# Optimization experiments

Measured on AMD Instinct MI355X. Metric: run time of the kernel, lower is better.

## Reference

```python
import jax, jax.numpy as jnp
import numpy as np

# Dims (Boltz MSA layer defaults)
S, N = 512, 384          # MSA depth, tokens
C_M, C_Z = 64, 128       # msa dim, pair dim
C_OPM = 32               # outer-product-mean hidden
H, DH = 8, 32            # heads, head_dim (H*DH == 256)
EPS = 1e-5


def _ln(x, w, b):
    mu = jnp.mean(x, axis=-1, keepdims=True)
    var = jnp.mean(jnp.square(x - mu), axis=-1, keepdims=True)
    return (x - mu) * jax.lax.rsqrt(var + EPS) * w + b


def setup_inputs() -> dict:
    key = jax.random.key(0)
    ks = iter(jax.random.split(key, 32))

    def p(*shape):
        return jax.random.normal(next(ks), shape, jnp.float32) * 0.02

    return {
        "m": jax.random.normal(next(ks), (1, S, N, C_M), jnp.float32),
        "z": jax.random.normal(next(ks), (1, N, N, C_Z), jnp.float32),
        # PairWeightedAveraging params
        "pwa_norm_m_w": jnp.ones((C_M,), jnp.float32),
        "pwa_norm_m_b": jnp.zeros((C_M,), jnp.float32),
        "pwa_norm_z_w": jnp.ones((C_Z,), jnp.float32),
        "pwa_norm_z_b": jnp.zeros((C_Z,), jnp.float32),
        "pwa_wm": p(C_M, H * DH),
        "pwa_wg": p(C_M, H * DH),
        "pwa_wz": p(C_Z, H),
        "pwa_wo": p(H * DH, C_M),
        # MSA Transition (SwiGLU, expansion 4)
        "tr_norm_w": jnp.ones((C_M,), jnp.float32),
        "tr_norm_b": jnp.zeros((C_M,), jnp.float32),
        "tr_w1": p(C_M, 4 * C_M),
        "tr_w2": p(C_M, 4 * C_M),
        "tr_w3": p(4 * C_M, C_M),
        # OuterProductMean params
        "opm_norm_w": jnp.ones((C_M,), jnp.float32),
        "opm_norm_b": jnp.zeros((C_M,), jnp.float32),
        "opm_wa": p(C_M, C_OPM),
        "opm_wb": p(C_M, C_OPM),
        "opm_wo": p(C_OPM * C_OPM, C_Z),
        "opm_bo": jnp.zeros((C_Z,), jnp.float32),
    }


def reference(m, z,
              pwa_norm_m_w, pwa_norm_m_b, pwa_norm_z_w, pwa_norm_z_b,
              pwa_wm, pwa_wg, pwa_wz, pwa_wo,
              tr_norm_w, tr_norm_b, tr_w1, tr_w2, tr_w3,
              opm_norm_w, opm_norm_b, opm_wa, opm_wb, opm_wo, opm_bo):
    m0 = m[0]   # [S, N, C_M]
    z0 = z[0]   # [N, N, C_Z]

    # --- Pair-weighted averaging (gated, per-head pair bias attention) ---
    mn = _ln(m0, pwa_norm_m_w, pwa_norm_m_b)
    zn = _ln(z0, pwa_norm_z_w, pwa_norm_z_b)
    b = zn @ pwa_wz                      # [N(i), N(j), H]
    w = jax.nn.softmax(b, axis=1)        # normalize over keys j
    v = (mn @ pwa_wm).reshape(S, N, H, DH)
    o = jnp.einsum('ijh,sjhd->sihd', w, v)           # [S, N, H, DH]
    g = jax.nn.sigmoid(mn @ pwa_wg).reshape(S, N, H, DH)
    pwa = (o * g).reshape(S, N, H * DH) @ pwa_wo     # [S, N, C_M]
    m1 = m0 + pwa

    # --- MSA transition (SwiGLU) ---
    tn = _ln(m1, tr_norm_w, tr_norm_b)
    m2 = m1 + (jax.nn.silu(tn @ tr_w1) * (tn @ tr_w2)) @ tr_w3

    # --- Outer product mean: MSA -> pair update ---
    on = _ln(m2, opm_norm_w, opm_norm_b)
    a = on @ opm_wa                      # [S, N, C]
    bb = on @ opm_wb                     # [S, N, C]
    op = jnp.einsum('sic,sjd->ijcd', a, bb) / S      # [N, N, C, C]
    zu = op.reshape(N, N, C_OPM * C_OPM) @ opm_wo + opm_bo
    z1 = z0 + zu

    return m2[None], z1[None]
```

## Files before the change

kernel.cpp:

```cpp
#include <hip/hip_runtime.h>
#include <hip/hip_bf16.h>

#define S_DIM 512
#define N_DIM 384
#define CM 64
#define CZ 128
#define HEADS 8
#define DH 32
#define HD 256

typedef __hip_bfloat16 bf16;
typedef long long i64;
typedef __attribute__((ext_vector_type(8))) short bf16x8;
typedef __attribute__((ext_vector_type(4))) float f32x4;

__device__ __forceinline__ float bf2f(bf16 x) { return __bfloat162float(x); }
__device__ __forceinline__ bf16 f2bf(float x) { return __float2bfloat16(x); }
__device__ __forceinline__ short f2bs(float x) {
  bf16 h = __float2bfloat16(x);
  return *reinterpret_cast<short*>(&h);
}

typedef __attribute__((address_space(3))) unsigned int lds_u32;
typedef __attribute__((address_space(1))) const unsigned int gbl_u32;
__device__ __forceinline__ void gl_lds16(const void* g, void* l) {
  __builtin_amdgcn_global_load_lds((gbl_u32*)g, (lds_u32*)l, 16, 0, 0);
}

__global__ __launch_bounds__(256) void k_wprep(const float* __restrict__ wm,
                                               const float* __restrict__ wg,
                                               const float* __restrict__ w1,
                                               const float* __restrict__ w2,
                                               const float* __restrict__ wpo,
                                               const float* __restrict__ w3,
                                               const float* __restrict__ wz,
                                               short* __restrict__ dst,
                                               short* __restrict__ wz_f) {
  if (blockIdx.x == 48) {
    int t = threadIdx.x;
    int ks = t >> 6, lane = t & 63, lg = lane >> 4, n = lane & 15;
    short out[8];
#pragma unroll
    for (int j = 0; j < 8; ++j) {
      int k = ks * 32 + lg * 8 + j;
      out[j] = (n < 8) ? f2bs(wz[k * 8 + n]) : (short)0;
    }
    *reinterpret_cast<float4*>(&wz_f[(size_t)t * 8]) =
        *reinterpret_cast<const float4*>(out);
    return;
  }
  int widx = blockIdx.x >> 3;
  const float* src;
  int N;
  if (widx == 0) { src = wm; N = 256; }
  else if (widx == 1) { src = wg; N = 256; }
  else if (widx == 2) { src = w1; N = 256; }
  else if (widx == 3) { src = w2; N = 256; }
  else if (widx == 4) { src = wpo; N = 64; }
  else { src = w3; N = 64; }
  int NF = N >> 4;
  int tg = ((blockIdx.x & 7) << 8) | threadIdx.x;
  int frag = tg >> 6, lane = tg & 63, lg = lane >> 4, l15 = lane & 15;
  int ks = frag / NF, nf = frag - ks * NF;
  short out[8];
#pragma unroll
  for (int j = 0; j < 8; ++j)
    out[j] = f2bs(src[(size_t)(ks * 32 + lg * 8 + j) * N + nf * 16 + l15]);
  *reinterpret_cast<float4*>(&dst[((size_t)widx << 14) + ((size_t)tg << 3)]) =
      *reinterpret_cast<const float4*>(out);
}

__global__ __launch_bounds__(256) void k_zb(const float* __restrict__ z,
                                            const float* __restrict__ w,
                                            const float* __restrict__ b,
                                            const short* __restrict__ wz_f,
                                            float* __restrict__ logits) {
  int blk = blockIdx.x;
  int i = blk / 6, j0 = (blk % 6) * 64;
  __shared__ __align__(16) char zl[16384];
  int t = threadIdx.x, wave = t >> 6, lane = t & 63;
  int lg = lane >> 4, l15 = lane & 15;
  float w0 = w[lane], w1 = w[lane + 64], b0 = b[lane], b1 = b[lane + 64];
  int rwb = wave * 16;
  const float* zbase = z + ((size_t)i * N_DIM + j0 + rwb) * CZ;
  for (int rr = 0; rr < 16; ++rr) {
    int row = rwb + rr;
    const float* zr = zbase + (size_t)rr * CZ;
    float v0 = zr[lane], v1 = zr[lane + 64];
    float s = v0 + v1, sq = v0 * v0 + v1 * v1;
#pragma unroll
    for (int off = 32; off; off >>= 1) {
      s += __shfl_xor(s, off);
      sq += __shfl_xor(sq, off);
    }
    float mu = s * (1.0f / CZ);
    float var = sq * (1.0f / CZ) - mu * mu;
    float rs = rsqrtf(var + 1e-5f);
    int sw = (row & 7) << 4;
    *reinterpret_cast<short*>(zl + row * 256 + ((2 * lane) ^ sw)) =
        f2bs((v0 - mu) * rs * w0 + b0);
    *reinterpret_cast<short*>(zl + row * 256 + ((2 * (lane + 64)) ^ sw)) =
        f2bs((v1 - mu) * rs * w1 + b1);
  }
  __syncthreads();
  f32x4 acc = (f32x4){0.f, 0.f, 0.f, 0.f};
  int arow = rwb + l15;
  int asw = (arow & 7) << 4;
#pragma unroll
  for (int ks = 0; ks < 4; ++ks) {
    bf16x8 a = *reinterpret_cast<const bf16x8*>(
        zl + arow * 256 + (((ks * 32 + lg * 8) * 2) ^ asw));
    bf16x8 bfr = *reinterpret_cast<const bf16x8*>(wz_f + ((size_t)ks * 64 + lane) * 8);
    acc = __builtin_amdgcn_mfma_f32_16x16x32_bf16(a, bfr, acc, 0, 0, 0);
  }
  if (l15 < 8) {
    int j = j0 + rwb + lg * 4;
    float4 o4;
    o4.x = acc[0]; o4.y = acc[1]; o4.z = acc[2]; o4.w = acc[3];
    *reinterpret_cast<float4*>(logits + ((size_t)i * 8 + l15) * N_DIM + j) = o4;
  }
}

__global__ __launch_bounds__(128) void k_softmax(const float* __restrict__ wb,
                                                 short* __restrict__ w8) {
  int row = blockIdx.x;
  int i = row >> 3, h = row & 7;
  const float* p = wb + (size_t)row * N_DIM;
  int t = threadIdx.x;
  float a0 = p[t], a1 = p[t + 128], a2 = p[t + 256];
  float mx = fmaxf(a0, fmaxf(a1, a2));
  __shared__ float red[2], red2[2];
#pragma unroll
  for (int off = 32; off; off >>= 1) mx = fmaxf(mx, __shfl_xor(mx, off));
  if ((t & 63) == 0) red[t >> 6] = mx;
  __syncthreads();
  mx = fmaxf(red[0], red[1]);
  float e0 = __expf(a0 - mx), e1 = __expf(a1 - mx), e2 = __expf(a2 - mx);
  float s = e0 + e1 + e2;
#pragma unroll
  for (int off = 32; off; off >>= 1) s += __shfl_xor(s, off);
  if ((t & 63) == 0) red2[t >> 6] = s;
  __syncthreads();
  float inv = 1.0f / (red2[0] + red2[1]);
  short* wr = w8 + ((size_t)h * N_DIM + i) * N_DIM;
  wr[t] = f2bs(e0 * inv);
  wr[t + 128] = f2bs(e1 * inv);
  wr[t + 256] = f2bs(e2 * inv);
}

__global__ __launch_bounds__(256, 1) void k_vgemm(const float* __restrict__ m0,
                                                  const float* __restrict__ nw,
                                                  const float* __restrict__ nb,
                                                  const short* __restrict__ wm_f,
                                                  short* __restrict__ vT) {
  int blk = blockIdx.x;
  int sblk = blk / 6, j0 = (blk % 6) * 64;
  __shared__ short vt[256 * 64];
  int t = threadIdx.x, wave = t >> 6, lane = t & 63;
  int lg = lane >> 4, l15 = lane & 15;
  size_t rb = (size_t)sblk * N_DIM + j0;
  int rw0 = wave * 16;
  const float* mrow = m0 + (rb + rw0 + l15) * CM;
  float4 x0 = *reinterpret_cast<const float4*>(mrow + lg * 8);
  float4 x1 = *reinterpret_cast<const float4*>(mrow + lg * 8 + 4);
  float4 x2 = *reinterpret_cast<const float4*>(mrow + 32 + lg * 8);
  float4 x3 = *reinterpret_cast<const float4*>(mrow + 32 + lg * 8 + 4);
  float s = x0.x + x0.y + x0.z + x0.w + x1.x + x1.y + x1.z + x1.w +
            x2.x + x2.y + x2.z + x2.w + x3.x + x3.y + x3.z + x3.w;
  float sq = x0.x * x0.x + x0.y * x0.y + x0.z * x0.z + x0.w * x0.w +
             x1.x * x1.x + x1.y * x1.y + x1.z * x1.z + x1.w * x1.w +
             x2.x * x2.x + x2.y * x2.y + x2.z * x2.z + x2.w * x2.w +
             x3.x * x3.x + x3.y * x3.y + x3.z * x3.z + x3.w * x3.w;
  s += __shfl_xor(s, 16); s += __shfl_xor(s, 32);
  sq += __shfl_xor(sq, 16); sq += __shfl_xor(sq, 32);
  float mu = s * (1.0f / CM);
  float var = sq * (1.0f / CM) - mu * mu;
  float rs = rsqrtf(var + 1e-5f);
  float4 g0 = *reinterpret_cast<const float4*>(nw + lg * 8);
  float4 g1 = *reinterpret_cast<const float4*>(nw + lg * 8 + 4);
  float4 g2 = *reinterpret_cast<const float4*>(nw + 32 + lg * 8);
  float4 g3 = *reinterpret_cast<const float4*>(nw + 32 + lg * 8 + 4);
  float4 c0 = *reinterpret_cast<const float4*>(nb + lg * 8);
  float4 c1 = *reinterpret_cast<const float4*>(nb + lg * 8 + 4);
  float4 c2 = *reinterpret_cast<const float4*>(nb + 32 + lg * 8);
  float4 c3 = *reinterpret_cast<const float4*>(nb + 32 + lg * 8 + 4);
  short av[16];
  av[0] = f2bs((x0.x - mu) * rs * g0.x + c0.x);
  av[1] = f2bs((x0.y - mu) * rs * g0.y + c0.y);
  av[2] = f2bs((x0.z - mu) * rs * g0.z + c0.z);
  av[3] = f2bs((x0.w - mu) * rs * g0.w + c0.w);
  av[4] = f2bs((x1.x - mu) * rs * g1.x + c1.x);
  av[5] = f2bs((x1.y - mu) * rs * g1.y + c1.y);
  av[6] = f2bs((x1.z - mu) * rs * g1.z + c1.z);
  av[7] = f2bs((x1.w - mu) * rs * g1.w + c1.w);
  av[8] = f2bs((x2.x - mu) * rs * g2.x + c2.x);
  av[9] = f2bs((x2.y - mu) * rs * g2.y + c2.y);
  av[10] = f2bs((x2.z - mu) * rs * g2.z + c2.z);
  av[11] = f2bs((x2.w - mu) * rs * g2.w + c2.w);
  av[12] = f2bs((x3.x - mu) * rs * g3.x + c3.x);
  av[13] = f2bs((x3.y - mu) * rs * g3.y + c3.y);
  av[14] = f2bs((x3.z - mu) * rs * g3.z + c3.z);
  av[15] = f2bs((x3.w - mu) * rs * g3.w + c3.w);
  bf16x8 a0 = *reinterpret_cast<const bf16x8*>(&av[0]);
  bf16x8 a1 = *reinterpret_cast<const bf16x8*>(&av[8]);
  f32x4 acc[16];
#pragma unroll
  for (int nf = 0; nf < 16; ++nf) acc[nf] = (f32x4){0.f, 0.f, 0.f, 0.f};
#pragma unroll
  for (int nf = 0; nf < 16; ++nf) {
    bf16x8 b0 = *reinterpret_cast<const bf16x8*>(wm_f + ((size_t)nf * 64 + lane) * 8);
    bf16x8 b1 = *reinterpret_cast<const bf16x8*>(wm_f + ((size_t)(16 + nf) * 64 + lane) * 8);
    acc[nf] = __builtin_amdgcn_mfma_f32_16x16x32_bf16(a0, b0, acc[nf], 0, 0, 0);
    acc[nf] = __builtin_amdgcn_mfma_f32_16x16x32_bf16(a1, b1, acc[nf], 0, 0, 0);
  }
#pragma unroll
  for (int nf = 0; nf < 16; ++nf)
#pragma unroll
    for (int r = 0; r < 4; ++r) {
      int jl = rw0 + lg * 4 + r;
      int hd = nf * 16 + l15;
      vt[hd * 64 + jl] = f2bs(acc[nf][r]);
    }
  __syncthreads();
  int h = t >> 5, d = t & 31;
  size_t gbase = ((size_t)h * 16384 + (size_t)sblk * 32 + d) * 384 + j0;
#pragma unroll
  for (int q = 0; q < 8; ++q)
    *reinterpret_cast<float4*>(&vT[gbase + q * 8]) =
        *reinterpret_cast<const float4*>(&vt[t * 64 + q * 8]);
}

__global__ __launch_bounds__(256, 2) void k_ogemm(const short* __restrict__ w8,
                                                  const short* __restrict__ vT,
                                                  bf16* __restrict__ o) {
  int h = blockIdx.y;
  int u = blockIdx.x;
  int gid = (u & 7) * 24 + (u >> 3);
  int nb = gid / 3, ib = gid % 3;
  int i0 = ib * 128;
  __shared__ __align__(16) char lds8[49152];
  char* LW = lds8;
  char* LV = lds8 + 16384;
  int t = threadIdx.x, wave = t >> 6, lane = t & 63;
  int lg = lane >> 4, l15 = lane & 15;
  f32x4 acc[8][4];
#pragma unroll
  for (int a = 0; a < 8; ++a)
#pragma unroll
    for (int b = 0; b < 4; ++b) acc[a][b] = (f32x4){0.f, 0.f, 0.f, 0.f};
  const short* Wb = w8 + ((size_t)h * N_DIM + i0) * N_DIM;
  const short* Vb = vT + ((size_t)h * 16384 + (size_t)nb * 256) * N_DIM;

  auto STAGE = [&](int buf, int kt) {
    int j0 = kt * 32;
#pragma unroll
    for (int q = 0; q < 2; ++q) {
      int c = t + q * 256;
      int ri = c >> 2, s = c & 3;
      gl_lds16(Wb + (size_t)ri * N_DIM + j0 + ((s ^ (ri & 3)) << 3),
               LW + buf * 8192 + c * 16);
    }
#pragma unroll
    for (int q = 0; q < 4; ++q) {
      int c = t + q * 256;
      int rn = c >> 2, s = c & 3;
      gl_lds16(Vb + (size_t)rn * N_DIM + j0 + ((s ^ (rn & 3)) << 3),
               LV + buf * 16384 + c * 16);
    }
  };

  STAGE(0, 0);
  __syncthreads();
  for (int kt = 0; kt < 12; ++kt) {
    int cur = kt & 1;
    if (kt < 11) STAGE(cur ^ 1, kt + 1);
    bf16x8 bfr[4];
#pragma unroll
    for (int fn = 0; fn < 4; ++fn) {
      int nl = wave * 64 + fn * 16 + l15;
      bfr[fn] = *reinterpret_cast<const bf16x8*>(
          LV + cur * 16384 + nl * 64 + ((lg * 16) ^ ((nl & 3) << 4)));
    }
#pragma unroll
    for (int fm = 0; fm < 8; ++fm) {
      int il = fm * 16 + l15;
      bf16x8 af = *reinterpret_cast<const bf16x8*>(
          LW + cur * 8192 + il * 64 + ((lg * 16) ^ ((il & 3) << 4)));
#pragma unroll
      for (int fn = 0; fn < 4; ++fn)
        acc[fm][fn] = __builtin_amdgcn_mfma_f32_16x16x32_bf16(
            af, bfr[fn], acc[fm][fn], 0, 0, 0);
    }
    __syncthreads();
  }
#pragma unroll
  for (int fm = 0; fm < 8; ++fm)
#pragma unroll
    for (int fn = 0; fn < 4; ++fn)
#pragma unroll
      for (int r = 0; r < 4; ++r) {
        int i = i0 + fm * 16 + lg * 4 + r;
        int n = nb * 256 + wave * 64 + fn * 16 + l15;
        int s = n >> 5, d = n & 31;
        o[((size_t)s * N_DIM + i) * HD + h * DH + d] = f2bf(acc[fm][fn][r]);
      }
}

#define OSTR 264
__global__ __launch_bounds__(256, 1) void k_pwa_out(const float* __restrict__ m0,
                                                    const bf16* __restrict__ o,
                                                    const float* __restrict__ nw,
                                                    const float* __restrict__ nb,
                                                    const short* __restrict__ wg_f,
                                                    const short* __restrict__ wpo_f,
                                                    float* __restrict__ m1out) {
  int blk = blockIdx.x;
  int sblk = blk / 6, j0 = (blk % 6) * 64;
  __shared__ __align__(16) short olds[64 * OSTR];
  __shared__ __align__(16) char hlds[32768];
  int t = threadIdx.x, wave = t >> 6, lane = t & 63;
  int lg = lane >> 4, l15 = lane & 15;
  size_t rb0 = (size_t)sblk * N_DIM + j0;
  size_t rb = rb0 + wave * 16;
#pragma unroll
  for (int q = 0; q < 8; ++q) {
    int f = t + q * 256;
    int row = f >> 5, pos = f & 31;
    *reinterpret_cast<float4*>(&olds[row * OSTR + pos * 8]) =
        *reinterpret_cast<const float4*>((const short*)o + (rb0 + row) * HD + pos * 8);
  }
  const float* mrow = m0 + (rb + l15) * CM;
  float4 x0 = *reinterpret_cast<const float4*>(mrow + lg * 8);
  float4 x1 = *reinterpret_cast<const float4*>(mrow + lg * 8 + 4);
  float4 x2 = *reinterpret_cast<const float4*>(mrow + 32 + lg * 8);
  float4 x3 = *reinterpret_cast<const float4*>(mrow + 32 + lg * 8 + 4);
  float s = x0.x + x0.y + x0.z + x0.w + x1.x + x1.y + x1.z + x1.w +
            x2.x + x2.y + x2.z + x2.w + x3.x + x3.y + x3.z + x3.w;
  float sq = x0.x * x0.x + x0.y * x0.y + x0.z * x0.z + x0.w * x0.w +
             x1.x * x1.x + x1.y * x1.y + x1.z * x1.z + x1.w * x1.w +
             x2.x * x2.x + x2.y * x2.y + x2.z * x2.z + x2.w * x2.w +
             x3.x * x3.x + x3.y * x3.y + x3.z * x3.z + x3.w * x3.w;
  s += __shfl_xor(s, 16); s += __shfl_xor(s, 32);
  sq += __shfl_xor(sq, 16); sq += __shfl_xor(sq, 32);
  float mu = s * (1.0f / CM);
  float var = sq * (1.0f / CM) - mu * mu;
  float rs = rsqrtf(var + 1e-5f);
  float4 g0 = *reinterpret_cast<const float4*>(nw + lg * 8);
  float4 g1 = *reinterpret_cast<const float4*>(nw + lg * 8 + 4);
  float4 g2 = *reinterpret_cast<const float4*>(nw + 32 + lg * 8);
  float4 g3 = *reinterpret_cast<const float4*>(nw + 32 + lg * 8 + 4);
  float4 c0 = *reinterpret_cast<const float4*>(nb + lg * 8);
  float4 c1 = *reinterpret_cast<const float4*>(nb + lg * 8 + 4);
  float4 c2 = *reinterpret_cast<const float4*>(nb + 32 + lg * 8);
  float4 c3 = *reinterpret_cast<const float4*>(nb + 32 + lg * 8 + 4);
  short av[16];
  av[0] = f2bs((x0.x - mu) * rs * g0.x + c0.x);
  av[1] = f2bs((x0.y - mu) * rs * g0.y + c0.y);
  av[2] = f2bs((x0.z - mu) * rs * g0.z + c0.z);
  av[3] = f2bs((x0.w - mu) * rs * g0.w + c0.w);
  av[4] = f2bs((x1.x - mu) * rs * g1.x + c1.x);
  av[5] = f2bs((x1.y - mu) * rs * g1.y + c1.y);
  av[6] = f2bs((x1.z - mu) * rs * g1.z + c1.z);
  av[7] = f2bs((x1.w - mu) * rs * g1.w + c1.w);
  av[8] = f2bs((x2.x - mu) * rs * g2.x + c2.x);
  av[9] = f2bs((x2.y - mu) * rs * g2.y + c2.y);
  av[10] = f2bs((x2.z - mu) * rs * g2.z + c2.z);
  av[11] = f2bs((x2.w - mu) * rs * g2.w + c2.w);
  av[12] = f2bs((x3.x - mu) * rs * g3.x + c3.x);
  av[13] = f2bs((x3.y - mu) * rs * g3.y + c3.y);
  av[14] = f2bs((x3.z - mu) * rs * g3.z + c3.z);
  av[15] = f2bs((x3.w - mu) * rs * g3.w + c3.w);
  bf16x8 a0 = *reinterpret_cast<const bf16x8*>(&av[0]);
  bf16x8 a1 = *reinterpret_cast<const bf16x8*>(&av[8]);
  f32x4 acc[16];
#pragma unroll
  for (int nf = 0; nf < 16; ++nf) acc[nf] = (f32x4){0.f, 0.f, 0.f, 0.f};
#pragma unroll
  for (int nf = 0; nf < 16; ++nf) {
    bf16x8 b0 = *reinterpret_cast<const bf16x8*>(wg_f + ((size_t)nf * 64 + lane) * 8);
    bf16x8 b1 = *reinterpret_cast<const bf16x8*>(wg_f + ((size_t)(16 + nf) * 64 + lane) * 8);
    acc[nf] = __builtin_amdgcn_mfma_f32_16x16x32_bf16(a0, b0, acc[nf], 0, 0, 0);
    acc[nf] = __builtin_amdgcn_mfma_f32_16x16x32_bf16(a1, b1, acc[nf], 0, 0, 0);
  }
  __syncthreads();
  char* hb = hlds + wave * 8192;
#pragma unroll
  for (int nf = 0; nf < 16; ++nf)
#pragma unroll
    for (int r = 0; r < 4; ++r) {
      int row = lg * 4 + r;
      float x = acc[nf][r];
      float g = 1.0f / (1.0f + __expf(-x));
      float ov = bf2f(*reinterpret_cast<const bf16*>(
          &olds[(wave * 16 + row) * OSTR + nf * 16 + l15]));
      *reinterpret_cast<short*>(
          hb + row * 512 + (((nf * 16 + l15) * 2) ^ ((row & 7) << 4))) = f2bs(g * ov);
    }
  __syncthreads();
  f32x4 acc3[4];
#pragma unroll
  for (int nf2 = 0; nf2 < 4; ++nf2) acc3[nf2] = (f32x4){0.f, 0.f, 0.f, 0.f};
#pragma unroll
  for (int ks2 = 0; ks2 < 8; ++ks2) {
    bf16x8 a2 = *reinterpret_cast<const bf16x8*>(
        hb + l15 * 512 + ((ks2 * 64 + lg * 16) ^ ((l15 & 7) << 4)));
#pragma unroll
    for (int nf2 = 0; nf2 < 4; ++nf2) {
      bf16x8 b = *reinterpret_cast<const bf16x8*>(
          wpo_f + ((size_t)(ks2 * 4 + nf2) * 64 + lane) * 8);
      acc3[nf2] = __builtin_amdgcn_mfma_f32_16x16x32_bf16(a2, b, acc3[nf2], 0, 0, 0);
    }
  }
#pragma unroll
  for (int nf2 = 0; nf2 < 4; ++nf2)
#pragma unroll
    for (int r = 0; r < 4; ++r) {
      size_t a = (rb + lg * 4 + r) * CM + nf2 * 16 + l15;
      m1out[a] = m0[a] + acc3[nf2][r];
    }
}

__global__ __launch_bounds__(256, 1) void k_transition(const float* __restrict__ nw,
                                                       const float* __restrict__ nb,
                                                       const short* __restrict__ w1_f,
                                                       const short* __restrict__ w2_f,
                                                       const short* __restrict__ w3_f,
                                                       float* __restrict__ mio) {
  __shared__ __align__(16) char hlds[32768];
  int t = threadIdx.x, wave = t >> 6, lane = t & 63;
  int lg = lane >> 4, l15 = lane & 15;
  size_t rb = (size_t)blockIdx.x * 64 + wave * 16;
  const float* mrow = mio + (rb + l15) * CM;
  float4 x0 = *reinterpret_cast<const float4*>(mrow + lg * 8);
  float4 x1 = *reinterpret_cast<const float4*>(mrow + lg * 8 + 4);
  float4 x2 = *reinterpret_cast<const float4*>(mrow + 32 + lg * 8);
  float4 x3 = *reinterpret_cast<const float4*>(mrow + 32 + lg * 8 + 4);
  float s = x0.x + x0.y + x0.z + x0.w + x1.x + x1.y + x1.z + x1.w +
            x2.x + x2.y + x2.z + x2.w + x3.x + x3.y + x3.z + x3.w;
  float sq = x0.x * x0.x + x0.y * x0.y + x0.z * x0.z + x0.w * x0.w +
             x1.x * x1.x + x1.y * x1.y + x1.z * x1.z + x1.w * x1.w +
             x2.x * x2.x + x2.y * x2.y + x2.z * x2.z + x2.w * x2.w +
             x3.x * x3.x + x3.y * x3.y + x3.z * x3.z + x3.w * x3.w;
  s += __shfl_xor(s, 16); s += __shfl_xor(s, 32);
  sq += __shfl_xor(sq, 16); sq += __shfl_xor(sq, 32);
  float mu = s * (1.0f / CM);
  float var = sq * (1.0f / CM) - mu * mu;
  float rs = rsqrtf(var + 1e-5f);
  float4 g0 = *reinterpret_cast<const float4*>(nw + lg * 8);
  float4 g1 = *reinterpret_cast<const float4*>(nw + lg * 8 + 4);
  float4 g2 = *reinterpret_cast<const float4*>(nw + 32 + lg * 8);
  float4 g3 = *reinterpret_cast<const float4*>(nw + 32 + lg * 8 + 4);
  float4 c0 = *reinterpret_cast<const float4*>(nb + lg * 8);
  float4 c1 = *reinterpret_cast<const float4*>(nb + lg * 8 + 4);
  float4 c2 = *reinterpret_cast<const float4*>(nb + 32 + lg * 8);
  float4 c3 = *reinterpret_cast<const float4*>(nb + 32 + lg * 8 + 4);
  short av[16];
  av[0] = f2bs((x0.x - mu) * rs * g0.x + c0.x);
  av[1] = f2bs((x0.y - mu) * rs * g0.y + c0.y);
  av[2] = f2bs((x0.z - mu) * rs * g0.z + c0.z);
  av[3] = f2bs((x0.w - mu) * rs * g0.w + c0.w);
  av[4] = f2bs((x1.x - mu) * rs * g1.x + c1.x);
  av[5] = f2bs((x1.y - mu) * rs * g1.y + c1.y);
  av[6] = f2bs((x1.z - mu) * rs * g1.z + c1.z);
  av[7] = f2bs((x1.w - mu) * rs * g1.w + c1.w);
  av[8] = f2bs((x2.x - mu) * rs * g2.x + c2.x);
  av[9] = f2bs((x2.y - mu) * rs * g2.y + c2.y);
  av[10] = f2bs((x2.z - mu) * rs * g2.z + c2.z);
  av[11] = f2bs((x2.w - mu) * rs * g2.w + c2.w);
  av[12] = f2bs((x3.x - mu) * rs * g3.x + c3.x);
  av[13] = f2bs((x3.y - mu) * rs * g3.y + c3.y);
  av[14] = f2bs((x3.z - mu) * rs * g3.z + c3.z);
  av[15] = f2bs((x3.w - mu) * rs * g3.w + c3.w);
  bf16x8 a0 = *reinterpret_cast<const bf16x8*>(&av[0]);
  bf16x8 a1 = *reinterpret_cast<const bf16x8*>(&av[8]);
  f32x4 acc1[16], acc2[16];
#pragma unroll
  for (int nf = 0; nf < 16; ++nf) {
    acc1[nf] = (f32x4){0.f, 0.f, 0.f, 0.f};
    acc2[nf] = (f32x4){0.f, 0.f, 0.f, 0.f};
  }
#pragma unroll
  for (int nf = 0; nf < 16; ++nf) {
    bf16x8 b10 = *reinterpret_cast<const bf16x8*>(w1_f + ((size_t)nf * 64 + lane) * 8);
    bf16x8 b11 = *reinterpret_cast<const bf16x8*>(w1_f + ((size_t)(16 + nf) * 64 + lane) * 8);
    acc1[nf] = __builtin_amdgcn_mfma_f32_16x16x32_bf16(a0, b10, acc1[nf], 0, 0, 0);
    acc1[nf] = __builtin_amdgcn_mfma_f32_16x16x32_bf16(a1, b11, acc1[nf], 0, 0, 0);
    bf16x8 b20 = *reinterpret_cast<const bf16x8*>(w2_f + ((size_t)nf * 64 + lane) * 8);
    bf16x8 b21 = *reinterpret_cast<const bf16x8*>(w2_f + ((size_t)(16 + nf) * 64 + lane) * 8);
    acc2[nf] = __builtin_amdgcn_mfma_f32_16x16x32_bf16(a0, b20, acc2[nf], 0, 0, 0);
    acc2[nf] = __builtin_amdgcn_mfma_f32_16x16x32_bf16(a1, b21, acc2[nf], 0, 0, 0);
  }
  char* hb = hlds + wave * 8192;
#pragma unroll
  for (int nf = 0; nf < 16; ++nf)
#pragma unroll
    for (int r = 0; r < 4; ++r) {
      int row = lg * 4 + r;
      float x = acc1[nf][r];
      float h = (x / (1.0f + __expf(-x))) * acc2[nf][r];
      *reinterpret_cast<short*>(
          hb + row * 512 + (((nf * 16 + l15) * 2) ^ ((row & 7) << 4))) = f2bs(h);
    }
  __syncthreads();
  f32x4 acc3[4];
#pragma unroll
  for (int nf2 = 0; nf2 < 4; ++nf2) acc3[nf2] = (f32x4){0.f, 0.f, 0.f, 0.f};
#pragma unroll
  for (int ks2 = 0; ks2 < 8; ++ks2) {
    bf16x8 a2 = *reinterpret_cast<const bf16x8*>(
        hb + l15 * 512 + ((ks2 * 64 + lg * 16) ^ ((l15 & 7) << 4)));
#pragma unroll
    for (int nf2 = 0; nf2 < 4; ++nf2) {
      bf16x8 b = *reinterpret_cast<const bf16x8*>(
          w3_f + ((size_t)(ks2 * 4 + nf2) * 64 + lane) * 8);
      acc3[nf2] = __builtin_amdgcn_mfma_f32_16x16x32_bf16(a2, b, acc3[nf2], 0, 0, 0);
    }
  }
#pragma unroll
  for (int nf2 = 0; nf2 < 4; ++nf2)
#pragma unroll
    for (int r = 0; r < 4; ++r) {
      size_t a = (rb + lg * 4 + r) * CM + nf2 * 16 + l15;
      mio[a] = mio[a] + acc3[nf2][r];
    }
}

__global__ __launch_bounds__(256) void k_opm_ab(const float* __restrict__ m2,
                                                const float* __restrict__ nw,
                                                const float* __restrict__ nb,
                                                const float* __restrict__ wa,
                                                const float* __restrict__ wb,
                                                unsigned char* __restrict__ at8,
                                                unsigned char* __restrict__ bt8) {
  int bix = blockIdx.x;
  int sg = bix / N_DIM;
  int i = bix - sg * N_DIM;
  __shared__ float on[64][65];
  __shared__ float wl[2][64][36];
  __shared__ float tl[2][32][65];
  int t = threadIdx.x, w = t >> 6, lane = t & 63;
  float gw = nw[lane], gb = nb[lane];
  for (int rr = 0; rr < 16; ++rr) {
    int sl = w * 16 + rr;
    float x = m2[((size_t)(sg * 64 + sl) * N_DIM + i) * CM + lane];
    float s = x, sq = x * x;
#pragma unroll
    for (int off = 32; off; off >>= 1) {
      s += __shfl_xor(s, off);
      sq += __shfl_xor(sq, off);
    }
    float mu = s * (1.0f / CM);
    float var = sq * (1.0f / CM) - mu * mu;
    float rs = rsqrtf(var + 1e-5f);
    on[sl][lane] = (x - mu) * rs * gw + gb;
  }
  for (int idx = t; idx < 2048; idx += 256) {
    int k = idx >> 5, c = idx & 31;
    wl[0][k][c] = wa[idx];
    wl[1][k][c] = wb[idx];
  }
  __syncthreads();
  int s = t >> 2, c0 = (t & 3) * 8;
  float accA[8], accB[8];
#pragma unroll
  for (int j = 0; j < 8; ++j) { accA[j] = 0.0f; accB[j] = 0.0f; }
  for (int k = 0; k < 64; ++k) {
    float ov = on[s][k];
#pragma unroll
    for (int j = 0; j < 8; ++j) {
      accA[j] += ov * wl[0][k][c0 + j];
      accB[j] += ov * wl[1][k][c0 + j];
    }
  }
#pragma unroll
  for (int j = 0; j < 8; ++j) {
    tl[0][c0 + j][s] = accA[j];
    tl[1][c0 + j][s] = accB[j];
  }
  __syncthreads();
  int cc = t >> 3, s8 = (t & 7) * 8;
  size_t ob = ((size_t)i * 32 + cc) * 512 + (size_t)sg * 64 + s8;
  unsigned int p0 = 0, p1 = 0;
  p0 = __builtin_amdgcn_cvt_pk_fp8_f32(tl[0][cc][s8 + 0], tl[0][cc][s8 + 1], p0, false);
  p0 = __builtin_amdgcn_cvt_pk_fp8_f32(tl[0][cc][s8 + 2], tl[0][cc][s8 + 3], p0, true);
  p1 = __builtin_amdgcn_cvt_pk_fp8_f32(tl[0][cc][s8 + 4], tl[0][cc][s8 + 5], p1, false);
  p1 = __builtin_amdgcn_cvt_pk_fp8_f32(tl[0][cc][s8 + 6], tl[0][cc][s8 + 7], p1, true);
  uint2 pa = {p0, p1};
  *reinterpret_cast<uint2*>(at8 + ob) = pa;
  p0 = 0; p1 = 0;
  p0 = __builtin_amdgcn_cvt_pk_fp8_f32(tl[1][cc][s8 + 0], tl[1][cc][s8 + 1], p0, false);
  p0 = __builtin_amdgcn_cvt_pk_fp8_f32(tl[1][cc][s8 + 2], tl[1][cc][s8 + 3], p0, true);
  p1 = __builtin_amdgcn_cvt_pk_fp8_f32(tl[1][cc][s8 + 4], tl[1][cc][s8 + 5], p1, false);
  p1 = __builtin_amdgcn_cvt_pk_fp8_f32(tl[1][cc][s8 + 6], tl[1][cc][s8 + 7], p1, true);
  uint2 pb = {p0, p1};
  *reinterpret_cast<uint2*>(bt8 + ob) = pb;
}

__global__ __launch_bounds__(256) void k_wot(const float* __restrict__ wo,
                                             short* __restrict__ wo_f) {
  int tg = blockIdx.x * 256 + threadIdx.x;
  int frag = tg >> 6, lane = tg & 63;
  int eblk = frag >> 5, kc = frag & 31;
  int e = eblk * 16 + (lane & 15);
  int kbase = kc * 32 + (lane >> 4) * 8;
  short out[8];
#pragma unroll
  for (int j = 0; j < 8; ++j) {
    int q = kbase + j;
    int row = ((q & 31) << 5) | (q >> 5);
    out[j] = f2bs(wo[(size_t)row * CZ + e]);
  }
  *reinterpret_cast<float4*>(&wo_f[(size_t)tg * 8]) =
      *reinterpret_cast<const float4*>(out);
}

__global__ __launch_bounds__(512, 2) void k_opm(const unsigned char* __restrict__ at8,
                                                const unsigned char* __restrict__ bt8,
                                                const short* __restrict__ wo_f,
                                                const float* __restrict__ bo,
                                                const float* __restrict__ z0,
                                                float* __restrict__ z1) {
  int g = blockIdx.x;
  int xcd = g & 7, u = g >> 3;
  int bn = u / 6;
  int bm = xcd * 6 + (u - bn * 6);
  __shared__ __align__(16) char lds8[66560];
  char* LA = lds8;
  char* LB = lds8 + 32768;
  int t = threadIdx.x, wave = t >> 6, lane = t & 63;
  int wm2 = wave >> 1, wn2 = wave & 1;
  int lg = lane >> 4, l15 = lane & 15;
  f32x4 acc[4][4];
#pragma unroll
  for (int a = 0; a < 4; ++a)
#pragma unroll
    for (int b = 0; b < 4; ++b) acc[a][b] = (f32x4){0.f, 0.f, 0.f, 0.f};
  const unsigned char* A = at8 + (size_t)bm * 131072;
  const unsigned char* B = bt8 + (size_t)bn * 65536;

  auto STAGE = [&](int buf, int kt) {
#pragma unroll
    for (int q = 0; q < 2; ++q) {
      int c = t + q * 512;
      int m = c >> 2, sl = c & 3;
      int so = kt * 64 + ((sl ^ ((m >> 1) & 3)) << 4);
      gl_lds16(A + (size_t)m * 512 + so, LA + buf * 16384 + c * 16);
    }
    {
      int m = t >> 2, sl = t & 3;
      int so = kt * 64 + ((sl ^ ((m >> 1) & 3)) << 4);
      gl_lds16(B + (size_t)m * 512 + so, LB + buf * 8192 + t * 16);
    }
  };

  STAGE(0, 0);
  __syncthreads();
  for (int kt = 0; kt < 8; ++kt) {
    int cur = kt & 1;
    if (kt < 7) STAGE(cur ^ 1, kt + 1);
#pragma unroll
    for (int ks = 0; ks < 2; ++ks) {
      int kk = ks * 32 + lg * 8;
      i64 bfr[4];
#pragma unroll
      for (int fn = 0; fn < 4; ++fn) {
        int n = wn2 * 64 + fn * 16 + l15;
        bfr[fn] = *reinterpret_cast<const i64*>(
            LB + cur * 8192 + n * 64 + (kk ^ (((n >> 1) & 3) << 4)));
      }
#pragma unroll
      for (int fm = 0; fm < 4; ++fm) {
        int m = wm2 * 64 + fm * 16 + l15;
        i64 af = *reinterpret_cast<const i64*>(
            LA + cur * 16384 + m * 64 + (kk ^ (((m >> 1) & 3) << 4)));
#pragma unroll
        for (int fn = 0; fn < 4; ++fn)
          acc[fm][fn] = __builtin_amdgcn_mfma_f32_16x16x32_fp8_fp8(
              af, bfr[fn], acc[fm][fn], 0, 0, 0);
      }
    }
    __syncthreads();
  }

  short* P = (short*)lds8;
  const float inv_s = 1.0f / 512.0f;
#pragma unroll
  for (int fm = 0; fm < 4; ++fm)
#pragma unroll
    for (int fn = 0; fn < 4; ++fn) {
      int m = wm2 * 64 + fm * 16 + lg * 4;
      int n = wn2 * 64 + fn * 16 + l15;
      int prow = (m >> 5) * 4 + (n >> 5);
      int cd2 = ((n & 31) << 5) | (m & 31);
      int pc = cd2 ^ (((cd2 >> 5) & 7) << 3);
      short pk[4];
#pragma unroll
      for (int r = 0; r < 4; ++r) pk[r] = f2bs(acc[fm][fn][r] * inv_s);
      *reinterpret_cast<uint2*>(P + prow * 1032 + pc) =
          *reinterpret_cast<const uint2*>(pk);
    }
  __syncthreads();

  int eblk = wave;
#pragma unroll
  for (int it = 0; it < 2; ++it) {
    f32x4 pacc = (f32x4){0.f, 0.f, 0.f, 0.f};
    for (int c0 = 0; c0 < 1024; c0 += 32) {
      int col = c0 + lg * 8;
      int pc = col ^ (((col >> 5) & 7) << 3);
      bf16x8 pa = *reinterpret_cast<const bf16x8*>(P + (it * 16 + l15) * 1032 + pc);
      bf16x8 pb = *reinterpret_cast<const bf16x8*>(
          wo_f + ((size_t)(eblk * 32 + (c0 >> 5)) * 64 + lane) * 8);
      pacc = __builtin_amdgcn_mfma_f32_16x16x32_bf16(pa, pb, pacc, 0, 0, 0);
    }
    int e = eblk * 16 + l15;
    float bov = bo[e];
#pragma unroll
    for (int r = 0; r < 4; ++r) {
      int prow = it * 16 + lg * 4 + r;
      int gi = bm * 8 + (prow >> 2), gj = bn * 4 + (prow & 3);
      size_t addr = ((size_t)gi * N_DIM + gj) * CZ + e;
      z1[addr] = z0[addr] + pacc[r] + bov;
    }
  }
}

extern "C" void kernel_launch(void* const* d_in, const int* in_sizes, int n_in,
                              void* d_out, int out_size, void* d_ws, size_t ws_size,
                              hipStream_t stream) {
  const float* m0 = (const float*)d_in[0];
  const float* z0 = (const float*)d_in[1];
  const float* pwa_nm_w = (const float*)d_in[2];
  const float* pwa_nm_b = (const float*)d_in[3];
  const float* pwa_nz_w = (const float*)d_in[4];
  const float* pwa_nz_b = (const float*)d_in[5];
  const float* pwa_wm = (const float*)d_in[6];
  const float* pwa_wg = (const float*)d_in[7];
  const float* pwa_wz = (const float*)d_in[8];
  const float* pwa_wo = (const float*)d_in[9];
  const float* tr_nw = (const float*)d_in[10];
  const float* tr_nb = (const float*)d_in[11];
  const float* tr_w1 = (const float*)d_in[12];
  const float* tr_w2 = (const float*)d_in[13];
  const float* tr_w3 = (const float*)d_in[14];
  const float* opm_nw = (const float*)d_in[15];
  const float* opm_nb = (const float*)d_in[16];
  const float* opm_wa = (const float*)d_in[17];
  const float* opm_wb = (const float*)d_in[18];
  const float* opm_wo = (const float*)d_in[19];
  const float* opm_bo = (const float*)d_in[20];

  char* ws = (char*)d_ws;
  float* wbuf = (float*)(ws + 25165824);
  short* vT = (short*)(ws + 29884416);
  bf16* o = (bf16*)(ws + 130547712);
  unsigned char* at8 = (unsigned char*)(ws + 29884416);
  unsigned char* bt8 = at8 + 6291456;
  short* wo_f = (short*)(ws + 55050240);
  short* wz_f = (short*)(ws + 55312384);

  float* m_out = (float*)d_out;
  float* z1 = m_out + (size_t)S_DIM * N_DIM * CM;
  short* packW = (short*)z1;
  short* wm_f = packW;
  short* wg_f = packW + 16384;
  short* w1_f = packW + 32768;
  short* w2_f = packW + 49152;
  short* wpo_f = packW + 65536;
  short* w3_f = packW + 81920;
  short* w8 = (short*)((char*)z1 + 262144);

  k_wprep<<<49, 256, 0, stream>>>(pwa_wm, pwa_wg, tr_w1, tr_w2, pwa_wo, tr_w3,
                                  pwa_wz, packW, wz_f);
  k_zb<<<2304, 256, 0, stream>>>(z0, pwa_nz_w, pwa_nz_b, wz_f, wbuf);
  k_softmax<<<3072, 128, 0, stream>>>(wbuf, w8);
  k_vgemm<<<3072, 256, 0, stream>>>(m0, pwa_nm_w, pwa_nm_b, wm_f, vT);
  k_ogemm<<<dim3(192, 8), 256, 0, stream>>>(w8, vT, o);
  k_pwa_out<<<3072, 256, 0, stream>>>(m0, o, pwa_nm_w, pwa_nm_b, wg_f, wpo_f, m_out);
  k_wot<<<64, 256, 0, stream>>>(opm_wo, wo_f);
  k_transition<<<3072, 256, 0, stream>>>(tr_nw, tr_nb, w1_f, w2_f, w3_f, m_out);
  k_opm_ab<<<3072, 256, 0, stream>>>(m_out, opm_nw, opm_nb, opm_wa, opm_wb, at8, bt8);
  k_opm<<<4608, 512, 0, stream>>>(at8, bt8, wo_f, opm_bo, z0, z1);
}
```

Measured before the change: 580.5 us.

## Pre-pack OPM fp8 operands in MFMA fragment order for contiguous staging

The producer kernel now writes the fp8 A and B operands of the outer-product GEMM directly in a per-tile, per-k-step, per-fragment lane order instead of a row-major [i*32+c][s] layout. The GEMM kernel then stages each k-tile with fully contiguous 16-byte global-to-LDS copies and reads MFMA fragments with a simple lane*8 offset, with no XOR swizzle arithmetic. This is meant to cut address computation and improve global load coalescing and LDS access patterns. The producer's stores become more scattered, and LDS bank conflicts may change since the swizzle is gone.

After: 565.3 us. 1.03x faster.

```diff
diff --git a/kernel.cpp b/kernel.cpp
--- a/kernel.cpp
+++ b/kernel.cpp
@@ -579,21 +579,26 @@
   }
   __syncthreads();
   int cc = t >> 3, s8 = (t & 7) * 8;
-  size_t ob = ((size_t)i * 32 + cc) * 512 + (size_t)sg * 64 + s8;
+  int lane8 = ((((s8 & 31) >> 3) * 16) + (cc & 15)) * 8;
+  int kg = sg * 2 + (s8 >> 5);
+  size_t obA = (size_t)(i >> 3) * 131072 + (size_t)kg * 8192 +
+               (size_t)((i & 7) * 2 + (cc >> 4)) * 512 + lane8;
+  size_t obB = (size_t)(i >> 2) * 65536 + (size_t)kg * 4096 +
+               (size_t)((i & 3) * 2 + (cc >> 4)) * 512 + lane8;
   unsigned int p0 = 0, p1 = 0;
   p0 = __builtin_amdgcn_cvt_pk_fp8_f32(tl[0][cc][s8 + 0], tl[0][cc][s8 + 1], p0, false);
   p0 = __builtin_amdgcn_cvt_pk_fp8_f32(tl[0][cc][s8 + 2], tl[0][cc][s8 + 3], p0, true);
   p1 = __builtin_amdgcn_cvt_pk_fp8_f32(tl[0][cc][s8 + 4], tl[0][cc][s8 + 5], p1, false);
   p1 = __builtin_amdgcn_cvt_pk_fp8_f32(tl[0][cc][s8 + 6], tl[0][cc][s8 + 7], p1, true);
   uint2 pa = {p0, p1};
-  *reinterpret_cast<uint2*>(at8 + ob) = pa;
+  *reinterpret_cast<uint2*>(at8 + obA) = pa;
   p0 = 0; p1 = 0;
   p0 = __builtin_amdgcn_cvt_pk_fp8_f32(tl[1][cc][s8 + 0], tl[1][cc][s8 + 1], p0, false);
   p0 = __builtin_amdgcn_cvt_pk_fp8_f32(tl[1][cc][s8 + 2], tl[1][cc][s8 + 3], p0, true);
   p1 = __builtin_amdgcn_cvt_pk_fp8_f32(tl[1][cc][s8 + 4], tl[1][cc][s8 + 5], p1, false);
   p1 = __builtin_amdgcn_cvt_pk_fp8_f32(tl[1][cc][s8 + 6], tl[1][cc][s8 + 7], p1, true);
   uint2 pb = {p0, p1};
-  *reinterpret_cast<uint2*>(bt8 + ob) = pb;
+  *reinterpret_cast<uint2*>(bt8 + obB) = pb;
 }
 
 __global__ __launch_bounds__(256) void k_wot(const float* __restrict__ wo,
@@ -639,18 +644,10 @@
   const unsigned char* B = bt8 + (size_t)bn * 65536;
 
   auto STAGE = [&](int buf, int kt) {
-#pragma unroll
-    for (int q = 0; q < 2; ++q) {
-      int c = t + q * 512;
-      int m = c >> 2, sl = c & 3;
-      int so = kt * 64 + ((sl ^ ((m >> 1) & 3)) << 4);
-      gl_lds16(A + (size_t)m * 512 + so, LA + buf * 16384 + c * 16);
-    }
-    {
-      int m = t >> 2, sl = t & 3;
-      int so = kt * 64 + ((sl ^ ((m >> 1) & 3)) << 4);
-      gl_lds16(B + (size_t)m * 512 + so, LB + buf * 8192 + t * 16);
-    }
+    gl_lds16(A + (size_t)kt * 16384 + t * 16, LA + buf * 16384 + t * 16);
+    gl_lds16(A + (size_t)kt * 16384 + 8192 + t * 16,
+             LA + buf * 16384 + 8192 + t * 16);
+    gl_lds16(B + (size_t)kt * 8192 + t * 16, LB + buf * 8192 + t * 16);
   };
 
   STAGE(0, 0);
@@ -658,21 +655,19 @@
   for (int kt = 0; kt < 8; ++kt) {
     int cur = kt & 1;
     if (kt < 7) STAGE(cur ^ 1, kt + 1);
+    const char* LAc = LA + cur * 16384;
+    const char* LBc = LB + cur * 8192;
 #pragma unroll
     for (int ks = 0; ks < 2; ++ks) {
-      int kk = ks * 32 + lg * 8;
       i64 bfr[4];
 #pragma unroll
-      for (int fn = 0; fn < 4; ++fn) {
-        int n = wn2 * 64 + fn * 16 + l15;
+      for (int fn = 0; fn < 4; ++fn)
         bfr[fn] = *reinterpret_cast<const i64*>(
-            LB + cur * 8192 + n * 64 + (kk ^ (((n >> 1) & 3) << 4)));
-      }
+            LBc + ks * 4096 + (wn2 * 4 + fn) * 512 + lane * 8);
 #pragma unroll
       for (int fm = 0; fm < 4; ++fm) {
-        int m = wm2 * 64 + fm * 16 + l15;
         i64 af = *reinterpret_cast<const i64*>(
-            LA + cur * 16384 + m * 64 + (kk ^ (((m >> 1) & 3) << 4)));
+            LAc + ks * 8192 + (wm2 * 4 + fm) * 512 + lane * 8);
 #pragma unroll
         for (int fn = 0; fn < 4; ++fn)
           acc[fm][fn] = __builtin_amdgcn_mfma_f32_16x16x32_fp8_fp8(
```
